# Kernel optimization log

Measured on AMD Instinct MI355X. Metric: run time of the kernel, lower is better.

## Reference

```python
import jax, jax.numpy as jnp
import numpy as np


def setup_inputs() -> dict:
    key = jax.random.key(0)
    k1, k2 = jax.random.split(key)
    N = 8192
    similarity = jax.random.normal(k1, (N, N), dtype=jnp.float32)
    text_to_img_mapping = jax.random.randint(k2, (N,), 0, N, dtype=jnp.int64)
    return {"similarity": similarity, "text_to_img_mapping": text_to_img_mapping}


def reference(similarity, text_to_img_mapping):
    n_text, n_img = similarity.shape
    rows = jnp.arange(n_text)
    # text->image CE: mean over text rows of -log_softmax(sim, axis=1)[i, map[i]]
    lsm_rows = jax.nn.log_softmax(similarity, axis=1)
    text_loss = -jnp.mean(lsm_rows[rows, text_to_img_mapping])
    # image->text CE with multi-hot soft targets mask[img, txt] = 1 iff map[txt] == img.
    # -sum(mask * log_softmax(sim.T, axis=1)) / n_img
    #   == -sum_i log_softmax(sim, axis=0)[i, map[i]] / n_img  (gather, no NxN mask)
    lsm_cols = jax.nn.log_softmax(similarity, axis=0)
    visual_loss = -jnp.sum(lsm_cols[rows, text_to_img_mapping]) / n_img
    return (text_loss + visual_loss) / 2.0
```

## Files before the change

### kernel.cpp

```cpp
#include <hip/hip_runtime.h>
#include <hip/hip_bf16.h>
#include <math.h>

#define N 8192
#define RB 32
#define T1 512
#define NRC (N / RB)
#define CPT 16


__global__ __launch_bounds__(T1)
void stage1(const float* __restrict__ sim, const long long* __restrict__ map,
            float* __restrict__ colS,
            float* __restrict__ blkPart) {
    const int tid = threadIdx.x;
    const int rc = blockIdx.x;
    const int rowBase = rc * RB;

    float cs[CPT];
    #pragma unroll
    for (int k = 0; k < CPT; ++k) cs[k] = 0.f;

    __shared__ float lrow[RB][T1];
    __shared__ float rowLog[RB];

    float gsum = 0.f;

    #pragma unroll 2
    for (int r = 0; r < RB; ++r) {
        const int row = rowBase + r;
        const float4* p = (const float4*)(sim + (size_t)row * N);
        float4 v0 = p[tid];
        float4 v1 = p[tid + T1];
        float4 v2 = p[tid + 2 * T1];
        float4 v3 = p[tid + 3 * T1];

        if (tid == 0) {
            int c = (int)map[row];
            gsum += sim[(size_t)row * N + c];
        }

        float e0 = __expf(v0.x), e1 = __expf(v0.y), e2 = __expf(v0.z), e3 = __expf(v0.w);
        float e4 = __expf(v1.x), e5 = __expf(v1.y), e6 = __expf(v1.z), e7 = __expf(v1.w);
        float e8 = __expf(v2.x), e9 = __expf(v2.y), eA = __expf(v2.z), eB = __expf(v2.w);
        float eC = __expf(v3.x), eD = __expf(v3.y), eE = __expf(v3.z), eF = __expf(v3.w);

        cs[0] += e0; cs[1] += e1; cs[2]  += e2; cs[3]  += e3;
        cs[4] += e4; cs[5] += e5; cs[6]  += e6; cs[7]  += e7;
        cs[8] += e8; cs[9] += e9; cs[10] += eA; cs[11] += eB;
        cs[12] += eC; cs[13] += eD; cs[14] += eE; cs[15] += eF;

        float rp = (((e0 + e1) + (e2 + e3)) + ((e4 + e5) + (e6 + e7)))
                 + (((e8 + e9) + (eA + eB)) + ((eC + eD) + (eE + eF)));
        lrow[r][tid] = rp;
    }
    __syncthreads();

    {
        const int r = tid >> 4, j = tid & 15;
        float s = 0.f;
        #pragma unroll
        for (int k = 0; k < T1 / 16; ++k)
            s += lrow[r][j + 16 * k];
        s += __shfl_xor(s, 1);
        s += __shfl_xor(s, 2);
        s += __shfl_xor(s, 4);
        s += __shfl_xor(s, 8);
        if (j == 0) rowLog[r] = __logf(s);
    }
    __syncthreads();

    if (tid == 0) {
        float b = -2.0f * gsum;
        #pragma unroll
        for (int r = 0; r < RB; ++r) b += rowLog[r];
        blkPart[rc] = b;
    }

    float4* outp = (float4*)(colS + (size_t)rc * N);
    outp[tid]          = make_float4(cs[0],  cs[1],  cs[2],  cs[3]);
    outp[tid + T1]     = make_float4(cs[4],  cs[5],  cs[6],  cs[7]);
    outp[tid + 2 * T1] = make_float4(cs[8],  cs[9],  cs[10], cs[11]);
    outp[tid + 3 * T1] = make_float4(cs[12], cs[13], cs[14], cs[15]);
}

__global__ __launch_bounds__(512)
void stage2(const float* __restrict__ colS, float* __restrict__ colLSE) {
    const int tid = threadIdx.x;
    const int cl = tid & 63;
    const int slice = tid >> 6;
    const int g = blockIdx.x * 64 + cl;

    float s = 0.f;
    #pragma unroll 4
    for (int k = 0; k < NRC / 8; ++k)
        s += colS[(size_t)(slice * (NRC / 8) + k) * N + g];

    __shared__ float lds[8][64];
    lds[slice][cl] = s;
    __syncthreads();

    if (tid < 64) {
        float t = 0.f;
        #pragma unroll
        for (int w = 0; w < 8; ++w) t += lds[w][tid];
        colLSE[blockIdx.x * 64 + tid] = __logf(t);
    }
}

__global__ __launch_bounds__(1024)
void stage3(const long long* __restrict__ map,
            const float* __restrict__ colLSE, const float* __restrict__ blkPart,
            float* __restrict__ out) {
    const int tid = threadIdx.x;
    float v = (tid < NRC) ? blkPart[tid] : 0.f;
    #pragma unroll
    for (int k = 0; k < N / 1024; ++k) {
        int i = k * 1024 + tid;
        v += colLSE[(int)map[i]];
    }
    #pragma unroll
    for (int off = 32; off >= 1; off >>= 1)
        v += __shfl_xor(v, off);
    __shared__ float red[16];
    const int wave = tid >> 6, lane = tid & 63;
    if (lane == 0) red[wave] = v;
    __syncthreads();
    if (tid == 0) {
        float t = 0.f;
        #pragma unroll
        for (int w = 0; w < 16; ++w) t += red[w];
        out[0] = t / (2.0f * (float)N);
    }
}

extern "C" void kernel_launch(void* const* d_in, const int* in_sizes, int n_in,
                              void* d_out, int out_size, void* d_ws, size_t ws_size,
                              hipStream_t stream) {
    const float* sim = (const float*)d_in[0];
    const long long* map = (const long long*)d_in[1];
    float* out = (float*)d_out;

    float* ws = (float*)d_ws;
    float* colS    = ws;
    float* colLSE  = colS + (size_t)NRC * N;
    float* blkPart = colLSE + N;

    stage1<<<NRC, T1, 0, stream>>>(sim, map, colS, blkPart);
    stage2<<<N / 64, 512, 0, stream>>>(colS, colLSE);
    stage3<<<1, 1024, 0, stream>>>(map, colLSE, blkPart, out);
}
```

Measured before the change: 56.02 us.

## Fuse final reduction into stage2 via last-block atomic counter

Removes the third kernel launch by having the last-finishing stage2 block, detected with an atomic counter and threadfences, do the gather-and-reduce. Stage2 now uses 256 blocks of 32 columns with 16 row slices instead of 128 blocks of 64 columns. Stage1 hoists the diagonal gather out of the row loop into a parallel per-thread load reduced by a wave shuffle, and writes its column sums before the block reduction. This trades one launch for atomic and fence overhead plus a serialized tail in the last block.

```diff
diff --git a/kernel.cpp b/kernel.cpp
--- a/kernel.cpp
+++ b/kernel.cpp
@@ -12,10 +12,20 @@
 __global__ __launch_bounds__(T1)
 void stage1(const float* __restrict__ sim, const long long* __restrict__ map,
             float* __restrict__ colS,
-            float* __restrict__ blkPart) {
+            float* __restrict__ blkPart,
+            unsigned int* __restrict__ done) {
     const int tid = threadIdx.x;
     const int rc = blockIdx.x;
     const int rowBase = rc * RB;
+
+    if (rc == 0 && tid == 0) *done = 0;
+
+    float gval = 0.f;
+    if (tid < RB) {
+        const int row = rowBase + tid;
+        const int c = (int)map[row];
+        gval = sim[(size_t)row * N + c];
+    }
 
     float cs[CPT];
     #pragma unroll
@@ -24,21 +34,13 @@
     __shared__ float lrow[RB][T1];
     __shared__ float rowLog[RB];
 
-    float gsum = 0.f;
-
     #pragma unroll 2
     for (int r = 0; r < RB; ++r) {
-        const int row = rowBase + r;
-        const float4* p = (const float4*)(sim + (size_t)row * N);
+        const float4* p = (const float4*)(sim + (size_t)(rowBase + r) * N);
         float4 v0 = p[tid];
         float4 v1 = p[tid + T1];
         float4 v2 = p[tid + 2 * T1];
         float4 v3 = p[tid + 3 * T1];
-
-        if (tid == 0) {
-            int c = (int)map[row];
-            gsum += sim[(size_t)row * N + c];
-        }
 
         float e0 = __expf(v0.x), e1 = __expf(v0.y), e2 = __expf(v0.z), e3 = __expf(v0.w);
         float e4 = __expf(v1.x), e5 = __expf(v1.y), e6 = __expf(v1.z), e7 = __expf(v1.w);
@@ -54,6 +56,13 @@
                  + (((e8 + e9) + (eA + eB)) + ((eC + eD) + (eE + eF)));
         lrow[r][tid] = rp;
     }
+
+    float4* outp = (float4*)(colS + (size_t)rc * N);
+    outp[tid]          = make_float4(cs[0],  cs[1],  cs[2],  cs[3]);
+    outp[tid + T1]     = make_float4(cs[4],  cs[5],  cs[6],  cs[7]);
+    outp[tid + 2 * T1] = make_float4(cs[8],  cs[9],  cs[10], cs[11]);
+    outp[tid + 3 * T1] = make_float4(cs[12], cs[13], cs[14], cs[15]);
+
     __syncthreads();
 
     {
@@ -68,68 +77,76 @@
         s += __shfl_xor(s, 8);
         if (j == 0) rowLog[r] = __logf(s);
     }
+
+    if (tid < 64) {
+        float g = gval;
+        #pragma unroll
+        for (int off = 32; off >= 1; off >>= 1)
+            g += __shfl_xor(g, off);
+        if (tid == 0) rowLog[0] += -2.0f * g;
+    }
     __syncthreads();
 
     if (tid == 0) {
-        float b = -2.0f * gsum;
+        float b = 0.f;
         #pragma unroll
         for (int r = 0; r < RB; ++r) b += rowLog[r];
         blkPart[rc] = b;
     }
-
-    float4* outp = (float4*)(colS + (size_t)rc * N);
-    outp[tid]          = make_float4(cs[0],  cs[1],  cs[2],  cs[3]);
-    outp[tid + T1]     = make_float4(cs[4],  cs[5],  cs[6],  cs[7]);
-    outp[tid + 2 * T1] = make_float4(cs[8],  cs[9],  cs[10], cs[11]);
-    outp[tid + 3 * T1] = make_float4(cs[12], cs[13], cs[14], cs[15]);
 }
 
 __global__ __launch_bounds__(512)
-void stage2(const float* __restrict__ colS, float* __restrict__ colLSE) {
+void stage2(const float* __restrict__ colS, const long long* __restrict__ map,
+            const float* __restrict__ blkPart, float* __restrict__ colLSE,
+            unsigned int* __restrict__ done, float* __restrict__ out) {
     const int tid = threadIdx.x;
-    const int cl = tid & 63;
-    const int slice = tid >> 6;
-    const int g = blockIdx.x * 64 + cl;
+    const int cl = tid & 31;
+    const int slice = tid >> 5;
+    const int g = blockIdx.x * 32 + cl;
 
     float s = 0.f;
     #pragma unroll 4
-    for (int k = 0; k < NRC / 8; ++k)
-        s += colS[(size_t)(slice * (NRC / 8) + k) * N + g];
+    for (int k = 0; k < NRC / 16; ++k)
+        s += colS[(size_t)(slice * (NRC / 16) + k) * N + g];
 
-    __shared__ float lds[8][64];
+    __shared__ float lds[16][32];
     lds[slice][cl] = s;
     __syncthreads();
 
-    if (tid < 64) {
+    if (tid < 32) {
         float t = 0.f;
         #pragma unroll
-        for (int w = 0; w < 8; ++w) t += lds[w][tid];
-        colLSE[blockIdx.x * 64 + tid] = __logf(t);
+        for (int w = 0; w < 16; ++w) t += lds[w][tid];
+        colLSE[blockIdx.x * 32 + tid] = __logf(t);
     }
-}
+    __syncthreads();
 
-__global__ __launch_bounds__(1024)
-void stage3(const long long* __restrict__ map,
-            const float* __restrict__ colLSE, const float* __restrict__ blkPart,
-            float* __restrict__ out) {
-    const int tid = threadIdx.x;
+    __shared__ bool amLast;
+    if (tid == 0) {
+        __threadfence();
+        amLast = (atomicAdd(done, 1u) == (unsigned)(gridDim.x - 1));
+    }
+    __syncthreads();
+    if (!amLast) return;
+
+    __threadfence();
     float v = (tid < NRC) ? blkPart[tid] : 0.f;
     #pragma unroll
-    for (int k = 0; k < N / 1024; ++k) {
-        int i = k * 1024 + tid;
+    for (int k = 0; k < N / 512; ++k) {
+        int i = k * 512 + tid;
         v += colLSE[(int)map[i]];
     }
     #pragma unroll
     for (int off = 32; off >= 1; off >>= 1)
         v += __shfl_xor(v, off);
-    __shared__ float red[16];
+    __shared__ float red[8];
     const int wave = tid >> 6, lane = tid & 63;
     if (lane == 0) red[wave] = v;
     __syncthreads();
     if (tid == 0) {
         float t = 0.f;
         #pragma unroll
-        for (int w = 0; w < 16; ++w) t += red[w];
+        for (int w = 0; w < 8; ++w) t += red[w];
         out[0] = t / (2.0f * (float)N);
     }
 }
@@ -145,8 +162,8 @@
     float* colS    = ws;
     float* colLSE  = colS + (size_t)NRC * N;
     float* blkPart = colLSE + N;
+    unsigned int* done = (unsigned int*)(blkPart + NRC);
 
-    stage1<<<NRC, T1, 0, stream>>>(sim, map, colS, blkPart);
-    stage2<<<N / 64, 512, 0, stream>>>(colS, colLSE);
-    stage3<<<1, 1024, 0, stream>>>(map, colLSE, blkPart, out);
+    stage1<<<NRC, T1, 0, stream>>>(sim, map, colS, blkPart, done);
+    stage2<<<NRC, 512, 0, stream>>>(colS, map, blkPart, colLSE, done, out);
 }
```

Result: slower. 62.05 us (+10.8%).
